# Kernel tuning notes

Measured on AMD Instinct MI355X. Metric: run time of the kernel, lower is better.

The kernel has to match this reference:

```python
import jax, jax.numpy as jnp
import numpy as np

NUM_CHANNELS = 64
IN_FEATURES = 256
OUT_FEATURES = 256
B = 128
N = 2048


def setup_inputs() -> dict:
    key = jax.random.key(0)
    k_x, k_c, k_w, k_b = jax.random.split(key, 4)
    x = jax.random.normal(k_x, (B, N, IN_FEATURES), dtype=jnp.float32)
    channels = jax.random.randint(k_c, (N,), 0, NUM_CHANNELS, dtype=jnp.int64)
    # kaiming_uniform_(a=sqrt(5)) over fan_in -> bound = 1/sqrt(fan_in)
    wb = 1.0 / np.sqrt(IN_FEATURES)
    weight = jax.random.uniform(k_w, (NUM_CHANNELS, OUT_FEATURES, IN_FEATURES),
                                dtype=jnp.float32, minval=-wb, maxval=wb)
    bias = jax.random.uniform(k_b, (NUM_CHANNELS, OUT_FEATURES),
                              dtype=jnp.float32, minval=-wb, maxval=wb)
    return {"x": x, "channels": channels, "weight": weight, "bias": bias}


def reference(x, channels, weight, bias):
    # Gather per-point weights/biases by channel id (shared across batch).
    w = weight[channels]          # [N, out, in]
    b = bias[channels]            # [N, out]
    # Equivalent to bmm over the point axis: [B,N,in] x [N,out,in] -> [B,N,out]
    y = jnp.einsum('bni,noi->bno', x, w)
    y = y + b                     # broadcast over batch
    y = jnp.tanh(y)               # activation=True
    y = y + x                     # residual mode 1 (out == in)
    return (y, channels)
```

## Files before the change

### kernel.cpp

```cpp
#include <hip/hip_runtime.h>
#include <hip/hip_bf16.h>


#define N_SZ 2048

typedef __attribute__((ext_vector_type(8))) __bf16 bf16x8;
typedef __attribute__((ext_vector_type(4))) float  f32x4;

__device__ __forceinline__ float bf2f(unsigned u16) {
    union { unsigned u; float f; } v; v.u = u16 << 16;
    return v.f;
}
__device__ __forceinline__ float tanh_fast(float s) {
    float a = fabsf(s);
    float t = __expf(-2.0f * a);
    float r = (1.0f - t) * __builtin_amdgcn_rcpf(1.0f + t);
    return __builtin_copysignf(r, s);
}
__device__ __forceinline__ bf16x8 cvt8(float4 a, float4 b) {
    bf16x8 v;
    v[0] = (__bf16)a.x; v[1] = (__bf16)a.y; v[2] = (__bf16)a.z; v[3] = (__bf16)a.w;
    v[4] = (__bf16)b.x; v[5] = (__bf16)b.y; v[6] = (__bf16)b.z; v[7] = (__bf16)b.w;
    return v;
}

__global__ __launch_bounds__(1024) void sort_kernel(const int* __restrict__ channels,
                                                    int* __restrict__ perm,
                                                    float* __restrict__ out_ch) {
    __shared__ int cnt[64], off[64];
    const int t = threadIdx.x;
    if (t < 64) cnt[t] = 0;
    __syncthreads();
    const int n0 = t, n1 = t + 1024;
    const int c0 = channels[n0], c1 = channels[n1];
    atomicAdd(&cnt[c0], 1);
    atomicAdd(&cnt[c1], 1);
    out_ch[n0] = (float)c0;
    out_ch[n1] = (float)c1;
    __syncthreads();
    if (t == 0) { int s = 0; for (int i = 0; i < 64; ++i) { off[i] = s; s += cnt[i]; } }
    __syncthreads();
    int p0 = atomicAdd(&off[c0], 1); perm[p0] = n0 | (c0 << 16);
    int p1 = atomicAdd(&off[c1], 1); perm[p1] = n1 | (c1 << 16);
}

__global__ __launch_bounds__(256) void wconv_kernel(const float* __restrict__ w,
                                                    unsigned short* __restrict__ wsW) {
    const size_t t = (size_t)blockIdx.x * 256 + threadIdx.x;
    const float* src = w + t * 8;
    float4 f0 = *(const float4*)(src);
    float4 f1 = *(const float4*)(src + 4);
    bf16x8 v = cvt8(f0, f1);
    *(bf16x8*)(wsW + t * 8) = v;
}

__global__ __launch_bounds__(512, 4) void channel_dense_kernel(
    const float* __restrict__ x, const int* __restrict__ perm,
    const unsigned short* __restrict__ wsW, const float* __restrict__ bias,
    float* __restrict__ y)
{
    __shared__ __align__(16) unsigned char sA[32768];

    const int g    = blockIdx.x;
    const int lg   = (g & 7) * 512 + (g >> 3);
    const int pv   = perm[lg >> 1];
    const int n    = pv & 0xffff;
    const int c    = pv >> 16;
    const int half = lg & 1;
    const int tid  = threadIdx.x;

    {
        const int r = tid >> 3;
        const int q = tid & 7;
        const float* xr = x + ((size_t)(half * 64 + r) * N_SZ + n) * 256 + q * 32;
        float4 la[8];
        #pragma unroll
        for (int j = 0; j < 8; ++j) la[j] = *(const float4*)(xr + j * 4);
        const int swz = (r & 7) << 4;
        #pragma unroll
        for (int j = 0; j < 4; ++j) {
            bf16x8 v = cvt8(la[2 * j], la[2 * j + 1]);
            *(bf16x8*)(sA + q * 4096 + ((r * 64 + j * 16) ^ swz)) = v;
        }
    }
    __syncthreads();

    const int lane = tid & 63, wv = tid >> 6;
    const int lr   = lane & 15, lg4 = lane >> 4;

    const unsigned short* wl = wsW + (((size_t)c * 256 + wv * 32 + lr) << 8) + lg4 * 8;
    const int lanebyte = (lr * 64 + lg4 * 16) ^ ((lr & 7) << 4);

    f32x4 acc[2][4] = {};

    #pragma unroll
    for (int kt = 0; kt < 8; ++kt) {
        bf16x8 wf0 = *(const bf16x8*)(wl + kt * 32);
        bf16x8 wf1 = *(const bf16x8*)(wl + 16 * 256 + kt * 32);
        bf16x8 xf[4];
        #pragma unroll
        for (int nb = 0; nb < 4; ++nb)
            xf[nb] = *(const bf16x8*)(sA + kt * 4096 + nb * 1024 + lanebyte);
        #pragma unroll
        for (int nb = 0; nb < 4; ++nb) {
            acc[0][nb] = __builtin_amdgcn_mfma_f32_16x16x32_bf16(wf0, xf[nb], acc[0][nb], 0, 0, 0);
            acc[1][nb] = __builtin_amdgcn_mfma_f32_16x16x32_bf16(wf1, xf[nb], acc[1][nb], 0, 0, 0);
        }
    }

    #pragma unroll
    for (int mo = 0; mo < 2; ++mo) {
        const int o0 = wv * 32 + mo * 16 + lg4 * 4;
        const float4 bv = *(const float4*)(bias + c * 256 + o0);
        #pragma unroll
        for (int nb = 0; nb < 4; ++nb) {
            const int rl = nb * 16 + lr;
            const int b  = half * 64 + rl;
            const int rbyte = wv * 4096 + ((rl * 64 + mo * 32 + lg4 * 8) ^ ((rl & 7) << 4));
            uint2 rv = *(const uint2*)(sA + rbyte);
            float4 o;
            o.x = tanh_fast(acc[mo][nb][0] + bv.x) + bf2f(rv.x & 0xffffu);
            o.y = tanh_fast(acc[mo][nb][1] + bv.y) + bf2f(rv.x >> 16);
            o.z = tanh_fast(acc[mo][nb][2] + bv.z) + bf2f(rv.y & 0xffffu);
            o.w = tanh_fast(acc[mo][nb][3] + bv.w) + bf2f(rv.y >> 16);
            *(float4*)(y + ((size_t)b * N_SZ + n) * 256 + o0) = o;
        }
    }
}

extern "C" void kernel_launch(void* const* d_in, const int* in_sizes, int n_in,
                              void* d_out, int out_size, void* d_ws, size_t ws_size,
                              hipStream_t stream) {
    const float* x        = (const float*)d_in[0];
    const int*   channels = (const int*)d_in[1];
    const float* weight   = (const float*)d_in[2];
    const float* bias     = (const float*)d_in[3];
    float* y = (float*)d_out;

    unsigned short* wsW = (unsigned short*)d_ws;
    int* perm = (int*)((unsigned char*)d_ws + (64u << 17));

    sort_kernel<<<dim3(1), dim3(1024), 0, stream>>>(
        channels, perm, y + (size_t)128 * N_SZ * 256);
    wconv_kernel<<<dim3(2048), dim3(256), 0, stream>>>(weight, wsW);
    channel_dense_kernel<<<dim3(4096), dim3(512), 0, stream>>>(
        x, perm, wsW, bias, y);
}
```

Baseline: 190.7 us.

## Split each point into four 32-row batch tiles with 256-thread blocks

The dense kernel now handles 32 batch rows per block instead of 64, using 4 waves of 64 output channels each, with half the LDS and twice as many blocks. Each wave loads four weight fragments per k-step and reuses two x fragments, and the LDS swizzle gains an extra XOR term to reduce bank conflicts. The aim is higher occupancy and better latency hiding in this memory-bound kernel. The cost is that each weight slice is reloaded from L2 by twice as many blocks.

```diff
diff --git a/kernel.cpp b/kernel.cpp
--- a/kernel.cpp
+++ b/kernel.cpp
@@ -54,33 +54,33 @@
     *(bf16x8*)(wsW + t * 8) = v;
 }
 
-__global__ __launch_bounds__(512, 4) void channel_dense_kernel(
+__global__ __launch_bounds__(256, 6) void channel_dense_kernel(
     const float* __restrict__ x, const int* __restrict__ perm,
     const unsigned short* __restrict__ wsW, const float* __restrict__ bias,
     float* __restrict__ y)
 {
-    __shared__ __align__(16) unsigned char sA[32768];
+    __shared__ __align__(16) unsigned char sA[16384];
 
-    const int g    = blockIdx.x;
-    const int lg   = (g & 7) * 512 + (g >> 3);
-    const int pv   = perm[lg >> 1];
-    const int n    = pv & 0xffff;
-    const int c    = pv >> 16;
-    const int half = lg & 1;
-    const int tid  = threadIdx.x;
+    const int g  = blockIdx.x;
+    const int lg = (g & 7) * 1024 + (g >> 3);
+    const int pv = perm[lg >> 2];
+    const int n  = pv & 0xffff;
+    const int c  = pv >> 16;
+    const int quarter = lg & 3;
+    const int tid = threadIdx.x;
 
     {
         const int r = tid >> 3;
         const int q = tid & 7;
-        const float* xr = x + ((size_t)(half * 64 + r) * N_SZ + n) * 256 + q * 32;
+        const float* xr = x + ((size_t)(quarter * 32 + r) * N_SZ + n) * 256 + q * 32;
         float4 la[8];
         #pragma unroll
         for (int j = 0; j < 8; ++j) la[j] = *(const float4*)(xr + j * 4);
-        const int swz = (r & 7) << 4;
+        const int swz = ((r & 7) << 4) ^ ((q & 3) << 4);
         #pragma unroll
         for (int j = 0; j < 4; ++j) {
             bf16x8 v = cvt8(la[2 * j], la[2 * j + 1]);
-            *(bf16x8*)(sA + q * 4096 + ((r * 64 + j * 16) ^ swz)) = v;
+            *(bf16x8*)(sA + q * 2048 + ((r * 64 + j * 16) ^ swz)) = v;
         }
     }
     __syncthreads();
@@ -88,35 +88,40 @@
     const int lane = tid & 63, wv = tid >> 6;
     const int lr   = lane & 15, lg4 = lane >> 4;
 
-    const unsigned short* wl = wsW + (((size_t)c * 256 + wv * 32 + lr) << 8) + lg4 * 8;
+    const unsigned short* wrow = wsW + (((size_t)c * 256 + wv * 64 + lr) << 8) + lg4 * 8;
     const int lanebyte = (lr * 64 + lg4 * 16) ^ ((lr & 7) << 4);
 
-    f32x4 acc[2][4] = {};
+    f32x4 acc[4][2] = {};
 
     #pragma unroll
     for (int kt = 0; kt < 8; ++kt) {
-        bf16x8 wf0 = *(const bf16x8*)(wl + kt * 32);
-        bf16x8 wf1 = *(const bf16x8*)(wl + 16 * 256 + kt * 32);
-        bf16x8 xf[4];
+        bf16x8 wf[4];
         #pragma unroll
-        for (int nb = 0; nb < 4; ++nb)
-            xf[nb] = *(const bf16x8*)(sA + kt * 4096 + nb * 1024 + lanebyte);
+        for (int mo = 0; mo < 4; ++mo)
+            wf[mo] = *(const bf16x8*)(wrow + mo * 4096 + kt * 32);
+        bf16x8 xf[2];
+        const int lb = lanebyte ^ ((kt & 3) << 4);
+        xf[0] = *(const bf16x8*)(sA + kt * 2048 + lb);
+        xf[1] = *(const bf16x8*)(sA + kt * 2048 + 1024 + lb);
         #pragma unroll
-        for (int nb = 0; nb < 4; ++nb) {
-            acc[0][nb] = __builtin_amdgcn_mfma_f32_16x16x32_bf16(wf0, xf[nb], acc[0][nb], 0, 0, 0);
-            acc[1][nb] = __builtin_amdgcn_mfma_f32_16x16x32_bf16(wf1, xf[nb], acc[1][nb], 0, 0, 0);
+        for (int mo = 0; mo < 4; ++mo) {
+            acc[mo][0] = __builtin_amdgcn_mfma_f32_16x16x32_bf16(wf[mo], xf[0], acc[mo][0], 0, 0, 0);
+            acc[mo][1] = __builtin_amdgcn_mfma_f32_16x16x32_bf16(wf[mo], xf[1], acc[mo][1], 0, 0, 0);
         }
     }
 
     #pragma unroll
-    for (int mo = 0; mo < 2; ++mo) {
-        const int o0 = wv * 32 + mo * 16 + lg4 * 4;
+    for (int mo = 0; mo < 4; ++mo) {
+        const int o0 = wv * 64 + mo * 16 + lg4 * 4;
         const float4 bv = *(const float4*)(bias + c * 256 + o0);
+        const int s     = o0 >> 5;
+        const int intra = (o0 & 31) * 2;
         #pragma unroll
-        for (int nb = 0; nb < 4; ++nb) {
+        for (int nb = 0; nb < 2; ++nb) {
             const int rl = nb * 16 + lr;
-            const int b  = half * 64 + rl;
-            const int rbyte = wv * 4096 + ((rl * 64 + mo * 32 + lg4 * 8) ^ ((rl & 7) << 4));
+            const int b  = quarter * 32 + rl;
+            const int rbyte = s * 2048 +
+                ((rl * 64 + intra) ^ ((rl & 7) << 4) ^ ((s & 3) << 4));
             uint2 rv = *(const uint2*)(sA + rbyte);
             float4 o;
             o.x = tanh_fast(acc[mo][nb][0] + bv.x) + bf2f(rv.x & 0xffffu);
@@ -143,6 +148,6 @@
     sort_kernel<<<dim3(1), dim3(1024), 0, stream>>>(
         channels, perm, y + (size_t)128 * N_SZ * 256);
     wconv_kernel<<<dim3(2048), dim3(256), 0, stream>>>(weight, wsW);
-    channel_dense_kernel<<<dim3(4096), dim3(512), 0, stream>>>(
+    channel_dense_kernel<<<dim3(8192), dim3(256), 0, stream>>>(
         x, perm, wsW, bias, y);
 }
```

Result: slower. 246.8 us (+29.4%).

## Persistent blocks process 16 sorted points with double-buffered LDS and cached weights

Applied to the files above, without the earlier changes.

The kernel now launches 512 blocks instead of 4096. Each block handles a quarter of the batch (32 rows) across 16 consecutive channel-sorted points. The next point's x tile is prefetched into registers and written to a second LDS buffer while the current one is computed. Weights and bias stay in registers and are reloaded only when the channel changes. This cuts the weight reloads and the per-block launch and sync overhead, but leaves fewer blocks to hide memory latency and adds a barrier on every iteration.

```diff
diff --git a/kernel.cpp b/kernel.cpp
--- a/kernel.cpp
+++ b/kernel.cpp
@@ -59,72 +59,112 @@
     const unsigned short* __restrict__ wsW, const float* __restrict__ bias,
     float* __restrict__ y)
 {
-    __shared__ __align__(16) unsigned char sA[32768];
+    __shared__ __align__(16) unsigned char sA[2][16384];
 
-    const int g    = blockIdx.x;
-    const int lg   = (g & 7) * 512 + (g >> 3);
-    const int pv   = perm[lg >> 1];
-    const int n    = pv & 0xffff;
-    const int c    = pv >> 16;
-    const int half = lg & 1;
+    const int g  = blockIdx.x;
+    const int lg = (g & 7) * 64 + (g >> 3);
+    const int chunk   = lg >> 2;
+    const int quarter = lg & 3;
     const int tid  = threadIdx.x;
-
-    {
-        const int r = tid >> 3;
-        const int q = tid & 7;
-        const float* xr = x + ((size_t)(half * 64 + r) * N_SZ + n) * 256 + q * 32;
-        float4 la[8];
-        #pragma unroll
-        for (int j = 0; j < 8; ++j) la[j] = *(const float4*)(xr + j * 4);
-        const int swz = (r & 7) << 4;
-        #pragma unroll
-        for (int j = 0; j < 4; ++j) {
-            bf16x8 v = cvt8(la[2 * j], la[2 * j + 1]);
-            *(bf16x8*)(sA + q * 4096 + ((r * 64 + j * 16) ^ swz)) = v;
-        }
-    }
-    __syncthreads();
-
     const int lane = tid & 63, wv = tid >> 6;
     const int lr   = lane & 15, lg4 = lane >> 4;
 
-    const unsigned short* wl = wsW + (((size_t)c * 256 + wv * 32 + lr) << 8) + lg4 * 8;
-    const int lanebyte = (lr * 64 + lg4 * 16) ^ ((lr & 7) << 4);
+    const int sr = tid >> 4;
+    const int sh = tid & 15;
+    const int s_slab = sh >> 1;
+    const int s_lin0 = sr * 64 + (sh & 1) * 32;
+    const int s_swz  = ((sr & 7) << 4) ^ ((s_slab & 3) << 4);
+    const int s_addr0 = s_slab * 2048 + ((s_lin0)      ^ s_swz);
+    const int s_addr1 = s_slab * 2048 + ((s_lin0 + 16) ^ s_swz);
 
-    f32x4 acc[2][4] = {};
+    float4 la0, la1, la2, la3;
+    auto stage_load = [&](int n_) {
+        const float* p = x + ((size_t)(quarter * 32 + sr) * N_SZ + n_) * 256 + sh * 16;
+        la0 = *(const float4*)(p);     la1 = *(const float4*)(p + 4);
+        la2 = *(const float4*)(p + 8); la3 = *(const float4*)(p + 12);
+    };
+    auto stage_write = [&](int buf) {
+        *(bf16x8*)(&sA[buf][s_addr0]) = cvt8(la0, la1);
+        *(bf16x8*)(&sA[buf][s_addr1]) = cvt8(la2, la3);
+    };
 
-    #pragma unroll
-    for (int kt = 0; kt < 8; ++kt) {
-        bf16x8 wf0 = *(const bf16x8*)(wl + kt * 32);
-        bf16x8 wf1 = *(const bf16x8*)(wl + 16 * 256 + kt * 32);
-        bf16x8 xf[4];
+    const int p0 = chunk * 16;
+
+    int pv_cur = perm[p0];
+    stage_load(pv_cur & 0xffff);
+    stage_write(0);
+    int pv_nxt = perm[p0 + 1];
+    stage_load(pv_nxt & 0xffff);
+    __syncthreads();
+
+    bf16x8 wreg[2][8];
+    float4 bv0, bv1;
+    int c_cur = -1;
+    int cur = 0;
+    const int o0 = wv * 32 + lg4 * 4;
+
+    for (int i = 0; i < 16; ++i) {
+        const int n = pv_cur & 0xffff;
+        const int c = pv_cur >> 16;
+        if (c != c_cur) {
+            c_cur = c;
+            const unsigned short* wl = wsW + (((size_t)c * 256 + wv * 32 + lr) << 8) + lg4 * 8;
+            #pragma unroll
+            for (int kt = 0; kt < 8; ++kt) {
+                wreg[0][kt] = *(const bf16x8*)(wl + kt * 32);
+                wreg[1][kt] = *(const bf16x8*)(wl + 16 * 256 + kt * 32);
+            }
+            bv0 = *(const float4*)(bias + c * 256 + o0);
+            bv1 = *(const float4*)(bias + c * 256 + o0 + 16);
+        }
+
+        f32x4 acc[2][2] = {};
         #pragma unroll
-        for (int nb = 0; nb < 4; ++nb)
-            xf[nb] = *(const bf16x8*)(sA + kt * 4096 + nb * 1024 + lanebyte);
+        for (int kt = 0; kt < 8; ++kt) {
+            const int lb = (lr * 64 + lg4 * 16) ^ ((lr & 7) << 4) ^ ((kt & 3) << 4);
+            bf16x8 xf0 = *(const bf16x8*)(&sA[cur][kt * 2048 + lb]);
+            bf16x8 xf1 = *(const bf16x8*)(&sA[cur][kt * 2048 + 1024 + lb]);
+            acc[0][0] = __builtin_amdgcn_mfma_f32_16x16x32_bf16(wreg[0][kt], xf0, acc[0][0], 0, 0, 0);
+            acc[0][1] = __builtin_amdgcn_mfma_f32_16x16x32_bf16(wreg[0][kt], xf1, acc[0][1], 0, 0, 0);
+            acc[1][0] = __builtin_amdgcn_mfma_f32_16x16x32_bf16(wreg[1][kt], xf0, acc[1][0], 0, 0, 0);
+            acc[1][1] = __builtin_amdgcn_mfma_f32_16x16x32_bf16(wreg[1][kt], xf1, acc[1][1], 0, 0, 0);
+        }
+
+        if (i < 15) {
+            stage_write(cur ^ 1);
+            if (i < 14) {
+                pv_cur = pv_nxt;
+                pv_nxt = perm[p0 + i + 2];
+                stage_load(pv_nxt & 0xffff);
+            } else {
+                pv_cur = pv_nxt;
+            }
+        }
+
         #pragma unroll
-        for (int nb = 0; nb < 4; ++nb) {
-            acc[0][nb] = __builtin_amdgcn_mfma_f32_16x16x32_bf16(wf0, xf[nb], acc[0][nb], 0, 0, 0);
-            acc[1][nb] = __builtin_amdgcn_mfma_f32_16x16x32_bf16(wf1, xf[nb], acc[1][nb], 0, 0, 0);
+        for (int mo = 0; mo < 2; ++mo) {
+            const float4 bv = mo ? bv1 : bv0;
+            const int oo    = o0 + mo * 16;
+            const int s     = oo >> 5;
+            const int intra = (oo & 31) * 2;
+            #pragma unroll
+            for (int nb = 0; nb < 2; ++nb) {
+                const int rl = nb * 16 + lr;
+                const int b  = quarter * 32 + rl;
+                const int rbyte = s * 2048 +
+                    ((rl * 64 + intra) ^ ((rl & 7) << 4) ^ ((s & 3) << 4));
+                uint2 rv = *(const uint2*)(&sA[cur][rbyte]);
+                float4 o;
+                o.x = tanh_fast(acc[mo][nb][0] + bv.x) + bf2f(rv.x & 0xffffu);
+                o.y = tanh_fast(acc[mo][nb][1] + bv.y) + bf2f(rv.x >> 16);
+                o.z = tanh_fast(acc[mo][nb][2] + bv.z) + bf2f(rv.y & 0xffffu);
+                o.w = tanh_fast(acc[mo][nb][3] + bv.w) + bf2f(rv.y >> 16);
+                *(float4*)(y + ((size_t)b * N_SZ + n) * 256 + oo) = o;
+            }
         }
-    }
 
-    #pragma unroll
-    for (int mo = 0; mo < 2; ++mo) {
-        const int o0 = wv * 32 + mo * 16 + lg4 * 4;
-        const float4 bv = *(const float4*)(bias + c * 256 + o0);
-        #pragma unroll
-        for (int nb = 0; nb < 4; ++nb) {
-            const int rl = nb * 16 + lr;
-            const int b  = half * 64 + rl;
-            const int rbyte = wv * 4096 + ((rl * 64 + mo * 32 + lg4 * 8) ^ ((rl & 7) << 4));
-            uint2 rv = *(const uint2*)(sA + rbyte);
-            float4 o;
-            o.x = tanh_fast(acc[mo][nb][0] + bv.x) + bf2f(rv.x & 0xffffu);
-            o.y = tanh_fast(acc[mo][nb][1] + bv.y) + bf2f(rv.x >> 16);
-            o.z = tanh_fast(acc[mo][nb][2] + bv.z) + bf2f(rv.y & 0xffffu);
-            o.w = tanh_fast(acc[mo][nb][3] + bv.w) + bf2f(rv.y >> 16);
-            *(float4*)(y + ((size_t)b * N_SZ + n) * 256 + o0) = o;
-        }
+        if (i < 15) __syncthreads();
+        cur ^= 1;
     }
 }
 
@@ -143,6 +183,6 @@
     sort_kernel<<<dim3(1), dim3(1024), 0, stream>>>(
         channels, perm, y + (size_t)128 * N_SZ * 256);
     wconv_kernel<<<dim3(2048), dim3(256), 0, stream>>>(weight, wsW);
-    channel_dense_kernel<<<dim3(4096), dim3(512), 0, stream>>>(
+    channel_dense_kernel<<<dim3(512), dim3(512), 0, stream>>>(
         x, perm, wsW, bias, y);
 }
```

New measurement: 181.8 us. 4.6% less time.
